# Kernel tuning notes

Measured on AMD Instinct MI355X. Metric: run time of the kernel, lower is better.

The kernel has to match this reference:

```python
import jax, jax.numpy as jnp
import numpy as np

NUM_HEADS = 8
N_POINTS = 9
OFFSET_SCALE = 4.0


def bilinear_sample(fmap_flat, xy, H, W):
    """fmap_flat: (BH, H*W, C) row-major spatial; xy: (BH, S, 2) pixel coords (x, y).
    grid_sample(mode='bilinear', padding_mode='zeros', align_corners=True) equivalent.
    Returns (BH, S, C)."""
    x, y = xy[..., 0], xy[..., 1]
    x0 = jnp.floor(x); y0 = jnp.floor(y)
    x1 = x0 + 1.0;    y1 = y0 + 1.0
    wx1 = x - x0; wx0 = 1.0 - wx1
    wy1 = y - y0; wy0 = 1.0 - wy1

    def corner(xi, yi, wgt):
        valid = (xi >= 0) & (xi <= W - 1) & (yi >= 0) & (yi <= H - 1)
        xi_c = jnp.clip(xi, 0, W - 1).astype(jnp.int32)
        yi_c = jnp.clip(yi, 0, H - 1).astype(jnp.int32)
        idx = yi_c * W + xi_c                                   # (BH, S)
        vals = jnp.take_along_axis(fmap_flat, idx[..., None], axis=1)  # (BH, S, C)
        return vals * (wgt * valid.astype(fmap_flat.dtype))[..., None]

    return (corner(x0, y0, wx0 * wy0) + corner(x1, y0, wx1 * wy0)
            + corner(x0, y1, wx0 * wy1) + corner(x1, y1, wx1 * wy1))


def setup_inputs() -> dict:
    key = jax.random.key(0)
    ks = jax.random.split(key, 10)
    B, N, D = 4, 6400, 256
    Hh, P = NUM_HEADS, N_POINTS
    s = 0.02
    return {
        "x":    jax.random.normal(ks[0], (B, N, D), dtype=jnp.float32),
        "Wq":   jax.random.normal(ks[1], (D, D), dtype=jnp.float32) * s,
        "bq":   jnp.zeros((D,), jnp.float32),
        "Woff": jax.random.normal(ks[2], (Hh * P * 2, D), dtype=jnp.float32) * s,
        "boff": jax.random.normal(ks[3], (Hh * P * 2,), dtype=jnp.float32) * s,
        "Wkv":  jax.random.normal(ks[4], (2 * D, D), dtype=jnp.float32) * s,
        "bkv":  jnp.zeros((2 * D,), jnp.float32),
        "Wout": jax.random.normal(ks[5], (D, D), dtype=jnp.float32) * s,
        "bout": jnp.zeros((D,), jnp.float32),
        "h": 40,
        "w": 160,
    }


def reference(x, Wq, bq, Woff, boff, Wkv, bkv, Wout, bout, h, w):
    B, N, D = x.shape
    H, P = NUM_HEADS, N_POINTS
    hd = D // H

    # queries: (B, H, N, hd)
    q = (x @ Wq.T + bq).reshape(B, N, H, hd).transpose(0, 2, 1, 3)

    # per-query per-head offsets in pixels: (B, N, H, P, 2) (dx, dy)
    offsets = jnp.tanh(x @ Woff.T + boff).reshape(B, N, H, P, 2) * OFFSET_SCALE

    # K/V feature maps via 1x1 conv == per-token linear; split heads, flat spatial
    kv = x @ Wkv.T + bkv                     # (B, N, 2D)
    k = kv[..., :D]
    v = kv[..., D:]
    k_flat = k.reshape(B, N, H, hd).transpose(0, 2, 1, 3).reshape(B * H, N, hd)
    v_flat = v.reshape(B, N, H, hd).transpose(0, 2, 1, 3).reshape(B * H, N, hd)

    # base pixel grid (x, y), row-major over (h, w)
    ys, xs = jnp.meshgrid(jnp.arange(h, dtype=x.dtype), jnp.arange(w, dtype=x.dtype), indexing="ij")
    base_xy = jnp.stack([xs, ys], axis=-1).reshape(N, 2)

    # sampling locations: (B, N, H, P, 2) -> (B*H, N*P, 2)
    sample_xy = base_xy[None, :, None, None, :] + offsets
    sample_xy = sample_xy.transpose(0, 2, 1, 3, 4).reshape(B * H, N * P, 2)

    sampled_k = bilinear_sample(k_flat, sample_xy, h, w).reshape(B, H, N, P, hd)
    sampled_v = bilinear_sample(v_flat, sample_xy, h, w).reshape(B, H, N, P, hd)

    logits = jnp.einsum("bhnd,bhnpd->bhnp", q, sampled_k) * (hd ** -0.5)
    attn = jax.nn.softmax(logits, axis=-1)
    out = jnp.einsum("bhnp,bhnpd->bhnd", attn, sampled_v)   # (B, H, N, hd)
    out = out.transpose(0, 2, 1, 3).reshape(B, N, D)
    return out @ Wout.T + bout
```

## Files before the change

kernel.cpp:

```cpp
#include <hip/hip_runtime.h>
#include <math.h>

#define BSZ    4
#define NTOK   6400
#define DMODEL 256
#define NHEAD  8
#define HDIM   32
#define NPTS   9
#define HSP    40
#define WSP    160
#define KDIM   256
#define MTOT   (BSZ*NTOK)

typedef short  short8  __attribute__((ext_vector_type(8)));
typedef float  floatx4 __attribute__((ext_vector_type(4)));

__device__ __forceinline__ ushort f2bf(float f) {
    uint u = __float_as_uint(f);
    u = (u + 0x7FFFu + ((u >> 16) & 1u)) >> 16;
    return (ushort)u;
}

__device__ __forceinline__ void unpack8(uint4 u, float* f) {
    f[0] = __uint_as_float(u.x << 16); f[1] = __uint_as_float(u.x & 0xFFFF0000u);
    f[2] = __uint_as_float(u.y << 16); f[3] = __uint_as_float(u.y & 0xFFFF0000u);
    f[4] = __uint_as_float(u.z << 16); f[5] = __uint_as_float(u.z & 0xFFFF0000u);
    f[6] = __uint_as_float(u.w << 16); f[7] = __uint_as_float(u.w & 0xFFFF0000u);
}

#define AS1C(p) ((const __attribute__((address_space(1))) void*)(p))
#define AS3(p)  ((__attribute__((address_space(3))) void*)(p))

__global__ __launch_bounds__(256) void cast_all(
    const float* __restrict__ x,   const float* __restrict__ Wq,
    const float* __restrict__ Woff,const float* __restrict__ Wkv,
    const float* __restrict__ Wout,
    ushort* __restrict__ xb, ushort* __restrict__ wqb, ushort* __restrict__ woffb,
    ushort* __restrict__ wkvb, ushort* __restrict__ woutb)
{
    const int bid = blockIdx.x;
    const float* src; ushort* dst; int base;
    if      (bid < 6400) { src = x;    dst = xb;    base = bid; }
    else if (bid < 6464) { src = Wq;   dst = wqb;   base = bid - 6400; }
    else if (bid < 6500) { src = Woff; dst = woffb; base = bid - 6464; }
    else if (bid < 6628) { src = Wkv;  dst = wkvb;  base = bid - 6500; }
    else                 { src = Wout; dst = woutb; base = bid - 6628; }
    const int i = base * 1024 + threadIdx.x * 4;
    float4 v = *(const float4*)(src + i);
    ushort4 o;
    o.x = f2bf(v.x); o.y = f2bf(v.y); o.z = f2bf(v.z); o.w = f2bf(v.w);
    *(ushort4*)(dst + i) = o;
}

template <int MODE>
__global__ __launch_bounds__(256) void gemm_bf16(
    const ushort* __restrict__ Xb,
    const ushort* __restrict__ Wb,
    const float* __restrict__ bias,
    void* __restrict__ Yv, void* __restrict__ Y2v,
    int Ncols)
{
    __shared__ ushort As[128 * 32];
    __shared__ ushort Bs[128 * 32];

    const int tid = threadIdx.x;
    const int block_m = blockIdx.y * 128;
    const int block_n = blockIdx.x * 128;
    const int wave = tid >> 6, lane = tid & 63;
    const int wm = (wave >> 1) * 64, wn = (wave & 1) * 64;
    const int l15 = lane & 15, quad = lane >> 4;

    const int srow = wave * 32 + (lane >> 2);
    const int scol = (lane & 3) * 8;

    const ushort* gA0 = Xb + (size_t)(block_m + srow) * KDIM + scol;
    const ushort* gA1 = gA0 + 16 * KDIM;
    int bc0 = block_n + srow, bc1 = bc0 + 16;
    if (MODE == 1) { bc0 = min(bc0, Ncols - 1); bc1 = min(bc1, Ncols - 1); }
    const ushort* gB0 = Wb + (size_t)bc0 * KDIM + scol;
    const ushort* gB1 = Wb + (size_t)bc1 * KDIM + scol;

    ushort* lA0 = &As[(wave * 32) * 32];
    ushort* lA1 = &As[(wave * 32 + 16) * 32];
    ushort* lB0 = &Bs[(wave * 32) * 32];
    ushort* lB1 = &Bs[(wave * 32 + 16) * 32];

    floatx4 acc[4][4];
    #pragma unroll
    for (int i = 0; i < 4; ++i)
        #pragma unroll
        for (int j = 0; j < 4; ++j) {
            acc[i][j][0] = 0.f; acc[i][j][1] = 0.f;
            acc[i][j][2] = 0.f; acc[i][j][3] = 0.f;
        }

    for (int k0 = 0; k0 < KDIM; k0 += 32) {
        __builtin_amdgcn_global_load_lds(AS1C(gA0 + k0), AS3(lA0), 16, 0, 0);
        __builtin_amdgcn_global_load_lds(AS1C(gA1 + k0), AS3(lA1), 16, 0, 0);
        __builtin_amdgcn_global_load_lds(AS1C(gB0 + k0), AS3(lB0), 16, 0, 0);
        __builtin_amdgcn_global_load_lds(AS1C(gB1 + k0), AS3(lB1), 16, 0, 0);
        __syncthreads();

        short8 af[4], bfr[4];
        #pragma unroll
        for (int f = 0; f < 4; ++f) {
            af[f]  = *(const short8*)&As[(wm + f * 16 + l15) * 32 + quad * 8];
            bfr[f] = *(const short8*)&Bs[(wn + f * 16 + l15) * 32 + quad * 8];
        }
        #pragma unroll
        for (int fm = 0; fm < 4; ++fm)
            #pragma unroll
            for (int fn = 0; fn < 4; ++fn)
                acc[fm][fn] = __builtin_amdgcn_mfma_f32_16x16x32_bf16(
                    af[fm], bfr[fn], acc[fm][fn], 0, 0, 0);
        __syncthreads();
    }

    #pragma unroll
    for (int fn = 0; fn < 4; ++fn) {
        const int col = block_n + wn + fn * 16 + l15;
        const float bcol = (MODE == 1 && col >= Ncols) ? 0.f : bias[col];
        #pragma unroll
        for (int fm = 0; fm < 4; ++fm) {
            #pragma unroll
            for (int r = 0; r < 4; ++r) {
                const int row = block_m + wm + fm * 16 + quad * 4 + r;
                const float val = acc[fm][fn][r] + bcol;
                if (MODE == 0) {
                    ((ushort*)Yv)[(size_t)row * DMODEL + col] = f2bf(val);
                } else if (MODE == 1) {
                    if (col < Ncols)
                        ((float*)Yv)[(size_t)row * 144 + col] = tanhf(val) * 4.0f;
                } else if (MODE == 2) {
                    const int b = row / NTOK, n = row % NTOK;
                    const int hh = (col & 255) >> 5, c = col & 31;
                    const size_t o = (((size_t)(b * NHEAD + hh)) * NTOK + n) * HDIM + c;
                    if (col < DMODEL) ((ushort*)Yv)[o]  = f2bf(val);
                    else              ((ushort*)Y2v)[o] = f2bf(val);
                } else {
                    ((float*)Yv)[(size_t)row * DMODEL + col] = val;
                }
            }
        }
    }
}

__global__ __launch_bounds__(256) void deform_attn(
    const ushort* __restrict__ qb,
    const float* __restrict__ off,
    const ushort* __restrict__ kfb,
    const ushort* __restrict__ vfb,
    ushort* __restrict__ attnb)
{
    const int lane = threadIdx.x & 63;
    const int token = blockIdx.x * 8 + (threadIdx.x >> 6) * 2 + (lane >> 5);
    const int h = (lane >> 2) & 7, lc = lane & 3;
    const int b = token / NTOK, n = token % NTOK;

    const uint4 qu = *(const uint4*)(qb + (size_t)token * DMODEL + h * HDIM + lc * 8);
    float q[8]; unpack8(qu, q);

    const float* ob = off + (size_t)token * 144 + h * (NPTS * 2);
    float2 offs[NPTS];
    #pragma unroll
    for (int p = 0; p < NPTS; ++p) offs[p] = *(const float2*)(ob + 2 * p);

    const float bx = (float)(n % WSP), by = (float)(n / WSP);
    const ushort* kb = kfb + (size_t)(b * NHEAD + h) * NTOK * HDIM + lc * 8;
    const ushort* vb = vfb + (size_t)(b * NHEAD + h) * NTOK * HDIM + lc * 8;

    float m = -INFINITY, s = 0.f;
    float o[8];
    #pragma unroll
    for (int c = 0; c < 8; ++c) o[c] = 0.f;

    #pragma unroll
    for (int p = 0; p < NPTS; ++p) {
        const float sx = bx + offs[p].x, sy = by + offs[p].y;
        const float fx0 = floorf(sx), fy0 = floorf(sy);
        const float wx1 = sx - fx0, wx0 = 1.0f - wx1;
        const float wy1 = sy - fy0, wy0 = 1.0f - wy1;
        const int ix0 = (int)fx0, iy0 = (int)fy0;
        const int ix1 = ix0 + 1, iy1 = iy0 + 1;
        const bool vx0 = (ix0 >= 0) & (ix0 <= WSP - 1);
        const bool vx1 = (ix1 >= 0) & (ix1 <= WSP - 1);
        const bool vy0 = (iy0 >= 0) & (iy0 <= HSP - 1);
        const bool vy1 = (iy1 >= 0) & (iy1 <= HSP - 1);
        const int cx0 = min(max(ix0, 0), WSP - 1);
        const int cx1 = min(max(ix1, 0), WSP - 1);
        const int cy0 = min(max(iy0, 0), HSP - 1);
        const int cy1 = min(max(iy1, 0), HSP - 1);
        const float w00 = wx0 * wy0 * (float)(vx0 && vy0);
        const float w10 = wx1 * wy0 * (float)(vx1 && vy0);
        const float w01 = wx0 * wy1 * (float)(vx0 && vy1);
        const float w11 = wx1 * wy1 * (float)(vx1 && vy1);
        const int i00 = (cy0 * WSP + cx0) * HDIM;
        const int i10 = (cy0 * WSP + cx1) * HDIM;
        const int i01 = (cy1 * WSP + cx0) * HDIM;
        const int i11 = (cy1 * WSP + cx1) * HDIM;

        const uint4 ku0 = *(const uint4*)(kb + i00);
        const uint4 ku1 = *(const uint4*)(kb + i10);
        const uint4 ku2 = *(const uint4*)(kb + i01);
        const uint4 ku3 = *(const uint4*)(kb + i11);
        const uint4 vu0 = *(const uint4*)(vb + i00);
        const uint4 vu1 = *(const uint4*)(vb + i10);
        const uint4 vu2 = *(const uint4*)(vb + i01);
        const uint4 vu3 = *(const uint4*)(vb + i11);

        float kc[8], d00 = 0.f, d10 = 0.f, d01 = 0.f, d11 = 0.f;
        unpack8(ku0, kc);
        #pragma unroll
        for (int c = 0; c < 8; ++c) d00 = fmaf(q[c], kc[c], d00);
        unpack8(ku1, kc);
        #pragma unroll
        for (int c = 0; c < 8; ++c) d10 = fmaf(q[c], kc[c], d10);
        unpack8(ku2, kc);
        #pragma unroll
        for (int c = 0; c < 8; ++c) d01 = fmaf(q[c], kc[c], d01);
        unpack8(ku3, kc);
        #pragma unroll
        for (int c = 0; c < 8; ++c) d11 = fmaf(q[c], kc[c], d11);

        float part = w00 * d00 + w10 * d10 + w01 * d01 + w11 * d11;
        part += __shfl_xor(part, 1, 64);
        part += __shfl_xor(part, 2, 64);
        const float l = part * 0.17677669529663687f;

        const float m1 = fmaxf(m, l);
        const float corr = __expf(m - m1);
        const float e = __expf(l - m1);
        s = fmaf(s, corr, e);
        m = m1;

        const float e00 = e * w00, e10 = e * w10, e01 = e * w01, e11 = e * w11;
        float v0[8], v1[8], v2[8], v3[8];
        unpack8(vu0, v0); unpack8(vu1, v1); unpack8(vu2, v2); unpack8(vu3, v3);
        #pragma unroll
        for (int c = 0; c < 8; ++c)
            o[c] = fmaf(o[c], corr,
                        fmaf(e00, v0[c], fmaf(e10, v1[c], fmaf(e01, v2[c], e11 * v3[c]))));
    }

    const float inv = 1.0f / s;
    uint4 ru;
    ru.x = (uint)f2bf(o[0] * inv) | ((uint)f2bf(o[1] * inv) << 16);
    ru.y = (uint)f2bf(o[2] * inv) | ((uint)f2bf(o[3] * inv) << 16);
    ru.z = (uint)f2bf(o[4] * inv) | ((uint)f2bf(o[5] * inv) << 16);
    ru.w = (uint)f2bf(o[6] * inv) | ((uint)f2bf(o[7] * inv) << 16);
    *(uint4*)(attnb + (size_t)token * DMODEL + h * HDIM + lc * 8) = ru;
}

extern "C" void kernel_launch(void* const* d_in, const int* in_sizes, int n_in,
                              void* d_out, int out_size, void* d_ws, size_t ws_size,
                              hipStream_t stream) {
    const float* x    = (const float*)d_in[0];
    const float* Wq   = (const float*)d_in[1];
    const float* bq   = (const float*)d_in[2];
    const float* Woff = (const float*)d_in[3];
    const float* boff = (const float*)d_in[4];
    const float* Wkv  = (const float*)d_in[5];
    const float* bkv  = (const float*)d_in[6];
    const float* Wout = (const float*)d_in[7];
    const float* bout = (const float*)d_in[8];

    ushort* xb    = (ushort*)d_ws;
    ushort* qb    = xb + (size_t)MTOT * DMODEL;
    float*  off   = (float*)(qb + (size_t)MTOT * DMODEL);
    ushort* kfb   = (ushort*)(off + (size_t)MTOT * 144);
    ushort* vfb   = kfb + (size_t)MTOT * DMODEL;
    ushort* wqb   = vfb + (size_t)MTOT * DMODEL;
    ushort* woffb = wqb + 65536;
    ushort* wkvb  = woffb + 36864;
    ushort* woutb = wkvb + 131072;
    ushort* attnb = xb;

    cast_all<<<dim3(6692), dim3(256), 0, stream>>>(x, Wq, Woff, Wkv, Wout,
                                                   xb, wqb, woffb, wkvb, woutb);

    gemm_bf16<0><<<dim3(2, 200), dim3(256), 0, stream>>>(xb, wqb, bq, qb, nullptr, 256);
    gemm_bf16<1><<<dim3(2, 200), dim3(256), 0, stream>>>(xb, woffb, boff, off, nullptr, 144);
    gemm_bf16<2><<<dim3(4, 200), dim3(256), 0, stream>>>(xb, wkvb, bkv, kfb, vfb, 512);
    deform_attn<<<dim3(3200), dim3(256), 0, stream>>>(qb, off, kfb, vfb, attnb);
    gemm_bf16<3><<<dim3(2, 200), dim3(256), 0, stream>>>(attnb, woutb, bout, d_out, nullptr, 256);
}
```

Baseline: 215.3 us.

## Fuse Q/offset/KV projections into one GEMM and interleave K/V layout

Concatates Wq, Woff and Wkv into one fused weight matrix so a single GEMM launch computes queries, offsets and keys/values, with a per-column epilogue routing results. K and V are stored interleaved per spatial position so each bilinear corner gather fetches K and V from one contiguous 128-byte span. The output projection uses a 128x64 tile to launch more blocks. The fused grid includes a mostly-empty last column tile, and the epilogue branches add per-column divergence.

```diff
diff --git a/kernel.cpp b/kernel.cpp
--- a/kernel.cpp
+++ b/kernel.cpp
@@ -11,6 +11,7 @@
 #define WSP    160
 #define KDIM   256
 #define MTOT   (BSZ*NTOK)
+#define NFUSED 912
 
 typedef short  short8  __attribute__((ext_vector_type(8)));
 typedef float  floatx4 __attribute__((ext_vector_type(4)));
@@ -35,16 +36,15 @@
     const float* __restrict__ x,   const float* __restrict__ Wq,
     const float* __restrict__ Woff,const float* __restrict__ Wkv,
     const float* __restrict__ Wout,
-    ushort* __restrict__ xb, ushort* __restrict__ wqb, ushort* __restrict__ woffb,
-    ushort* __restrict__ wkvb, ushort* __restrict__ woutb)
+    ushort* __restrict__ xb, ushort* __restrict__ wfused, ushort* __restrict__ woutb)
 {
     const int bid = blockIdx.x;
     const float* src; ushort* dst; int base;
-    if      (bid < 6400) { src = x;    dst = xb;    base = bid; }
-    else if (bid < 6464) { src = Wq;   dst = wqb;   base = bid - 6400; }
-    else if (bid < 6500) { src = Woff; dst = woffb; base = bid - 6464; }
-    else if (bid < 6628) { src = Wkv;  dst = wkvb;  base = bid - 6500; }
-    else                 { src = Wout; dst = woutb; base = bid - 6628; }
+    if      (bid < 6400) { src = x;    dst = xb;              base = bid; }
+    else if (bid < 6464) { src = Wq;   dst = wfused;          base = bid - 6400; }
+    else if (bid < 6500) { src = Woff; dst = wfused + 65536;  base = bid - 6464; }
+    else if (bid < 6628) { src = Wkv;  dst = wfused + 102400; base = bid - 6500; }
+    else                 { src = Wout; dst = woutb;           base = bid - 6628; }
     const int i = base * 1024 + threadIdx.x * 4;
     float4 v = *(const float4*)(src + i);
     ushort4 o;
@@ -52,13 +52,12 @@
     *(ushort4*)(dst + i) = o;
 }
 
-template <int MODE>
-__global__ __launch_bounds__(256) void gemm_bf16(
+__global__ __launch_bounds__(256) void gemm_fused(
     const ushort* __restrict__ Xb,
     const ushort* __restrict__ Wb,
-    const float* __restrict__ bias,
-    void* __restrict__ Yv, void* __restrict__ Y2v,
-    int Ncols)
+    const float* __restrict__ bq, const float* __restrict__ boff,
+    const float* __restrict__ bkv,
+    ushort* __restrict__ qb, float* __restrict__ off, ushort* __restrict__ kvb)
 {
     __shared__ ushort As[128 * 32];
     __shared__ ushort Bs[128 * 32];
@@ -75,8 +74,8 @@
 
     const ushort* gA0 = Xb + (size_t)(block_m + srow) * KDIM + scol;
     const ushort* gA1 = gA0 + 16 * KDIM;
-    int bc0 = block_n + srow, bc1 = bc0 + 16;
-    if (MODE == 1) { bc0 = min(bc0, Ncols - 1); bc1 = min(bc1, Ncols - 1); }
+    const int bc0 = min(block_n + srow, NFUSED - 1);
+    const int bc1 = min(block_n + srow + 16, NFUSED - 1);
     const ushort* gB0 = Wb + (size_t)bc0 * KDIM + scol;
     const ushort* gB1 = Wb + (size_t)bc1 * KDIM + scol;
 
@@ -119,27 +118,101 @@
     #pragma unroll
     for (int fn = 0; fn < 4; ++fn) {
         const int col = block_n + wn + fn * 16 + l15;
-        const float bcol = (MODE == 1 && col >= Ncols) ? 0.f : bias[col];
+        if (col >= NFUSED) continue;
+        const float bcol = (col < 256) ? bq[col]
+                         : (col < 400) ? boff[col - 256]
+                                       : bkv[col - 400];
         #pragma unroll
         for (int fm = 0; fm < 4; ++fm) {
             #pragma unroll
             for (int r = 0; r < 4; ++r) {
                 const int row = block_m + wm + fm * 16 + quad * 4 + r;
                 const float val = acc[fm][fn][r] + bcol;
-                if (MODE == 0) {
-                    ((ushort*)Yv)[(size_t)row * DMODEL + col] = f2bf(val);
-                } else if (MODE == 1) {
-                    if (col < Ncols)
-                        ((float*)Yv)[(size_t)row * 144 + col] = tanhf(val) * 4.0f;
-                } else if (MODE == 2) {
+                if (col < 256) {
+                    qb[(size_t)row * DMODEL + col] = f2bf(val);
+                } else if (col < 400) {
+                    off[(size_t)row * 144 + (col - 256)] = tanhf(val) * 4.0f;
+                } else {
+                    const int kc = col - 400;
                     const int b = row / NTOK, n = row % NTOK;
-                    const int hh = (col & 255) >> 5, c = col & 31;
-                    const size_t o = (((size_t)(b * NHEAD + hh)) * NTOK + n) * HDIM + c;
-                    if (col < DMODEL) ((ushort*)Yv)[o]  = f2bf(val);
-                    else              ((ushort*)Y2v)[o] = f2bf(val);
-                } else {
-                    ((float*)Yv)[(size_t)row * DMODEL + col] = val;
+                    const int hh = (kc >> 5) & 7, c = kc & 31;
+                    const int vo = (kc >= 256) ? 32 : 0;
+                    kvb[(((size_t)(b * NHEAD + hh)) * NTOK + n) * 64 + c + vo] = f2bf(val);
                 }
+            }
+        }
+    }
+}
+
+__global__ __launch_bounds__(256) void gemm_out(
+    const ushort* __restrict__ Xb,
+    const ushort* __restrict__ Wb,
+    const float* __restrict__ bias,
+    float* __restrict__ Y)
+{
+    __shared__ ushort As[128 * 32];
+    __shared__ ushort Bs[64 * 32];
+
+    const int tid = threadIdx.x;
+    const int block_m = blockIdx.y * 128;
+    const int block_n = blockIdx.x * 64;
+    const int wave = tid >> 6, lane = tid & 63;
+    const int wm = (wave & 1) * 64, wn = (wave >> 1) * 32;
+    const int l15 = lane & 15, quad = lane >> 4;
+
+    const int srow = wave * 32 + (lane >> 2);
+    const int scol = (lane & 3) * 8;
+    const int srowB = wave * 16 + (lane >> 2);
+
+    const ushort* gA0 = Xb + (size_t)(block_m + srow) * KDIM + scol;
+    const ushort* gA1 = gA0 + 16 * KDIM;
+    const ushort* gB  = Wb + (size_t)(block_n + srowB) * KDIM + scol;
+
+    ushort* lA0 = &As[(wave * 32) * 32];
+    ushort* lA1 = &As[(wave * 32 + 16) * 32];
+    ushort* lB  = &Bs[(wave * 16) * 32];
+
+    floatx4 acc[4][2];
+    #pragma unroll
+    for (int i = 0; i < 4; ++i)
+        #pragma unroll
+        for (int j = 0; j < 2; ++j) {
+            acc[i][j][0] = 0.f; acc[i][j][1] = 0.f;
+            acc[i][j][2] = 0.f; acc[i][j][3] = 0.f;
+        }
+
+    for (int k0 = 0; k0 < KDIM; k0 += 32) {
+        __builtin_amdgcn_global_load_lds(AS1C(gA0 + k0), AS3(lA0), 16, 0, 0);
+        __builtin_amdgcn_global_load_lds(AS1C(gA1 + k0), AS3(lA1), 16, 0, 0);
+        __builtin_amdgcn_global_load_lds(AS1C(gB  + k0), AS3(lB),  16, 0, 0);
+        __syncthreads();
+
+        short8 af[4], bfr[2];
+        #pragma unroll
+        for (int f = 0; f < 4; ++f)
+            af[f] = *(const short8*)&As[(wm + f * 16 + l15) * 32 + quad * 8];
+        #pragma unroll
+        for (int f = 0; f < 2; ++f)
+            bfr[f] = *(const short8*)&Bs[(wn + f * 16 + l15) * 32 + quad * 8];
+        #pragma unroll
+        for (int fm = 0; fm < 4; ++fm)
+            #pragma unroll
+            for (int fn = 0; fn < 2; ++fn)
+                acc[fm][fn] = __builtin_amdgcn_mfma_f32_16x16x32_bf16(
+                    af[fm], bfr[fn], acc[fm][fn], 0, 0, 0);
+        __syncthreads();
+    }
+
+    #pragma unroll
+    for (int fn = 0; fn < 2; ++fn) {
+        const int col = block_n + wn + fn * 16 + l15;
+        const float bcol = bias[col];
+        #pragma unroll
+        for (int fm = 0; fm < 4; ++fm) {
+            #pragma unroll
+            for (int r = 0; r < 4; ++r) {
+                const int row = block_m + wm + fm * 16 + quad * 4 + r;
+                Y[(size_t)row * DMODEL + col] = acc[fm][fn][r] + bcol;
             }
         }
     }
@@ -148,8 +221,7 @@
 __global__ __launch_bounds__(256) void deform_attn(
     const ushort* __restrict__ qb,
     const float* __restrict__ off,
-    const ushort* __restrict__ kfb,
-    const ushort* __restrict__ vfb,
+    const ushort* __restrict__ kvb,
     ushort* __restrict__ attnb)
 {
     const int lane = threadIdx.x & 63;
@@ -166,8 +238,7 @@
     for (int p = 0; p < NPTS; ++p) offs[p] = *(const float2*)(ob + 2 * p);
 
     const float bx = (float)(n % WSP), by = (float)(n / WSP);
-    const ushort* kb = kfb + (size_t)(b * NHEAD + h) * NTOK * HDIM + lc * 8;
-    const ushort* vb = vfb + (size_t)(b * NHEAD + h) * NTOK * HDIM + lc * 8;
+    const ushort* kb = kvb + (size_t)(b * NHEAD + h) * NTOK * 64 + lc * 8;
 
     float m = -INFINITY, s = 0.f;
     float o[8];
@@ -194,19 +265,19 @@
         const float w10 = wx1 * wy0 * (float)(vx1 && vy0);
         const float w01 = wx0 * wy1 * (float)(vx0 && vy1);
         const float w11 = wx1 * wy1 * (float)(vx1 && vy1);
-        const int i00 = (cy0 * WSP + cx0) * HDIM;
-        const int i10 = (cy0 * WSP + cx1) * HDIM;
-        const int i01 = (cy1 * WSP + cx0) * HDIM;
-        const int i11 = (cy1 * WSP + cx1) * HDIM;
+        const int i00 = (cy0 * WSP + cx0) * 64;
+        const int i10 = (cy0 * WSP + cx1) * 64;
+        const int i01 = (cy1 * WSP + cx0) * 64;
+        const int i11 = (cy1 * WSP + cx1) * 64;
 
         const uint4 ku0 = *(const uint4*)(kb + i00);
         const uint4 ku1 = *(const uint4*)(kb + i10);
         const uint4 ku2 = *(const uint4*)(kb + i01);
         const uint4 ku3 = *(const uint4*)(kb + i11);
-        const uint4 vu0 = *(const uint4*)(vb + i00);
-        const uint4 vu1 = *(const uint4*)(vb + i10);
-        const uint4 vu2 = *(const uint4*)(vb + i01);
-        const uint4 vu3 = *(const uint4*)(vb + i11);
+        const uint4 vu0 = *(const uint4*)(kb + i00 + 32);
+        const uint4 vu1 = *(const uint4*)(kb + i10 + 32);
+        const uint4 vu2 = *(const uint4*)(kb + i01 + 32);
+        const uint4 vu3 = *(const uint4*)(kb + i11 + 32);
 
         float kc[8], d00 = 0.f, d10 = 0.f, d01 = 0.f, d11 = 0.f;
         unpack8(ku0, kc);
@@ -264,23 +335,18 @@
     const float* Wout = (const float*)d_in[7];
     const float* bout = (const float*)d_in[8];
 
-    ushort* xb    = (ushort*)d_ws;
-    ushort* qb    = xb + (size_t)MTOT * DMODEL;
-    float*  off   = (float*)(qb + (size_t)MTOT * DMODEL);
-    ushort* kfb   = (ushort*)(off + (size_t)MTOT * 144);
-    ushort* vfb   = kfb + (size_t)MTOT * DMODEL;
-    ushort* wqb   = vfb + (size_t)MTOT * DMODEL;
-    ushort* woffb = wqb + 65536;
-    ushort* wkvb  = woffb + 36864;
-    ushort* woutb = wkvb + 131072;
-    ushort* attnb = xb;
+    ushort* xb     = (ushort*)d_ws;
+    ushort* qb     = xb + (size_t)MTOT * DMODEL;
+    float*  off    = (float*)(qb + (size_t)MTOT * DMODEL);
+    ushort* kvb    = (ushort*)(off + (size_t)MTOT * 144);
+    ushort* wfused = kvb + (size_t)MTOT * 512;
+    ushort* woutb  = wfused + NFUSED * KDIM;
+    ushort* attnb  = xb;
 
     cast_all<<<dim3(6692), dim3(256), 0, stream>>>(x, Wq, Woff, Wkv, Wout,
-                                                   xb, wqb, woffb, wkvb, woutb);
-
-    gemm_bf16<0><<<dim3(2, 200), dim3(256), 0, stream>>>(xb, wqb, bq, qb, nullptr, 256);
-    gemm_bf16<1><<<dim3(2, 200), dim3(256), 0, stream>>>(xb, woffb, boff, off, nullptr, 144);
-    gemm_bf16<2><<<dim3(4, 200), dim3(256), 0, stream>>>(xb, wkvb, bkv, kfb, vfb, 512);
-    deform_attn<<<dim3(3200), dim3(256), 0, stream>>>(qb, off, kfb, vfb, attnb);
-    gemm_bf16<3><<<dim3(2, 200), dim3(256), 0, stream>>>(attnb, woutb, bout, d_out, nullptr, 256);
-}
+                                                   xb, wfused, woutb);
+    gemm_fused<<<dim3(8, 200), dim3(256), 0, stream>>>(xb, wfused, bq, boff, bkv,
+                                                       qb, off, kvb);
+    deform_attn<<<dim3(3200), dim3(256), 0, stream>>>(qb, off, kvb, attnb);
+    gemm_out<<<dim3(4, 200), dim3(256), 0, stream>>>(attnb, woutb, bout, (float*)d_out);
+}
```

New measurement: 231.0 us. +7.3%, slower.
